# Optimization experiments

Hardware: AMD Instinct MI355X
Metric: run time of the kernel (lower is better)

The kernel has to match this reference:

```python
import jax, jax.numpy as jnp
import numpy as np

TOP_K = 8

def setup_inputs() -> dict:
    key = jax.random.key(0)
    k1, k2, k3, k4 = jax.random.split(key, 4)
    B, T, C, E = 4, 4096, 2048, 64
    x = jax.random.normal(k1, (B, T, C), dtype=jnp.float32)
    w_route = jax.random.normal(k2, (E, C), dtype=jnp.float32) * (C ** -0.5)
    w_noise = jax.random.normal(k3, (E, C), dtype=jnp.float32) * (C ** -0.5)
    noise = jax.random.normal(k4, (B, T, E), dtype=jnp.float32)
    return {"x": x, "w_route": w_route, "w_noise": w_noise, "noise": noise}

def reference(x, w_route, w_noise, noise):
    # logits = x @ W_route^T ; noise_logits = x @ W_noise^T  (bias-free Linears)
    logits = jnp.einsum('btc,ec->bte', x, w_route)
    noise_logits = jnp.einsum('btc,ec,->bte', x, w_noise, jnp.float32(1.0)) if False else jnp.einsum('btc,ec->bte', x, w_noise)
    noisy_logits = logits + noise * jax.nn.softplus(noise_logits)
    # top-k over experts, scatter into -inf tensor, then softmax
    topk_vals, indices = jax.lax.top_k(noisy_logits, TOP_K)  # (B,T,K)
    E = noisy_logits.shape[-1]
    in_topk = jax.nn.one_hot(indices, E, dtype=jnp.bool_).any(axis=-2)  # (B,T,E)
    sparse_logits = jnp.where(in_topk, noisy_logits, -jnp.inf)
    router_output = jax.nn.softmax(sparse_logits, axis=-1)
    return router_output, indices
```

## Files before the change

kernel.cpp:

```cpp
#include <hip/hip_runtime.h>
#include <math.h>


#define CDIM  2048
#define EDIM  64
#define NOUT  128
#define TOPK  8
#define BM    32
#define BKS   64
#define NSIT  (CDIM / BKS)
#define NKC   (CDIM / 32)
#define TAU   1e-3f
#define XPS   136

typedef __attribute__((ext_vector_type(8))) short bf16x8;
typedef __attribute__((ext_vector_type(4))) float f32x4;

__device__ __forceinline__ void split8(const float4 a, const float4 b,
                                       bf16x8& h8, bf16x8& l8) {
    const float vv[8] = {a.x, a.y, a.z, a.w, b.x, b.y, b.z, b.w};
    #pragma unroll
    for (int j = 0; j < 8; ++j) {
        const __bf16 h = (__bf16)vv[j];
        const __bf16 l = (__bf16)(vv[j] - (float)h);
        h8[j] = __builtin_bit_cast(short, h);
        l8[j] = __builtin_bit_cast(short, l);
    }
}

__global__ __launch_bounds__(256)
void convert_w(const float* __restrict__ wr, const float* __restrict__ wn,
               short* __restrict__ whi, short* __restrict__ wlo) {
    const int s    = (int)blockIdx.x * 256 + (int)threadIdx.x;
    const int lane = s & 63;
    const int cg   = (s >> 6) & 7;
    const int kc   = s >> 9;
    const int col  = cg * 16 + (lane & 15);
    const int k0   = kc * 32 + (lane >> 4) * 8;
    const float* src = (col < EDIM ? wr + (size_t)col * CDIM
                                   : wn + (size_t)(col - EDIM) * CDIM) + k0;
    const float4 a = *(const float4*)src;
    const float4 b = *(const float4*)(src + 4);
    bf16x8 h8, l8; split8(a, b, h8, l8);
    *(bf16x8*)(whi + (size_t)s * 8) = h8;
    *(bf16x8*)(wlo + (size_t)s * 8) = l8;
}

__global__ __launch_bounds__(256, 2)
void router_fused(const float* __restrict__ x,
                  const short* __restrict__ whi,
                  const short* __restrict__ wlo,
                  const float* __restrict__ w_route,
                  const float* __restrict__ w_noise,
                  const float* __restrict__ noise,
                  float* __restrict__ out_probs,
                  float* __restrict__ out_idx)
{
    __shared__ __align__(16) short xsh[2][BM][XPS];
    __shared__ __align__(16) float scr[BM][NOUT + 8];
    __shared__ __align__(16) float vals[4][64];
    __shared__ __align__(16) float srt[4][64];

    const int tid  = (int)threadIdx.x;
    const int lane = tid & 63;
    const int wid  = tid >> 6;
    const int wr   = wid >> 1;
    const int wc   = wid & 1;
    const int l15  = lane & 15;
    const int q8   = (lane >> 4) * 8;
    const int q4   = (lane >> 4) * 4;
    const int row0 = (int)blockIdx.x * BM;

    const int srow = tid >> 3;
    const int skk  = (tid & 7) * 8;
    const float* xsrc = x + (size_t)(row0 + srow) * CDIM + skk;

    f32x4 acc[4];
    #pragma unroll
    for (int nc = 0; nc < 4; ++nc)
        acc[nc] = (f32x4){0.f, 0.f, 0.f, 0.f};

    bf16x8 bh[2][4], bl[2][4];
    auto loadB = [&](int buf, int kc) {
        const int base = (kc * 8 + wc * 4) * 512 + lane * 8;
        #pragma unroll
        for (int nc = 0; nc < 4; ++nc) {
            bh[buf][nc] = *(const bf16x8*)(whi + base + nc * 512);
            bl[buf][nc] = *(const bf16x8*)(wlo + base + nc * 512);
        }
    };

    loadB(0, 0);
    {
        const float4 a = *(const float4*)xsrc;
        const float4 b = *(const float4*)(xsrc + 4);
        bf16x8 h8, l8; split8(a, b, h8, l8);
        *(bf16x8*)&xsh[0][srow][skk]      = h8;
        *(bf16x8*)&xsh[0][srow][64 + skk] = l8;
    }
    __syncthreads();

    #pragma unroll 2
    for (int sit = 0; sit < NSIT; ++sit) {
        const int  cur = sit & 1;
        const bool pf  = (sit + 1 < NSIT);
        const int  g0  = sit * 2;

        loadB(1, g0 + 1);
        float4 pa, pb;
        if (pf) {
            pa = *(const float4*)(xsrc + (sit + 1) * BKS);
            pb = *(const float4*)(xsrc + (sit + 1) * BKS + 4);
        }

        const short* ar = &xsh[cur][wr * 16 + l15][0];
        {
            const bf16x8 ah = *(const bf16x8*)(ar + q8);
            const bf16x8 al = *(const bf16x8*)(ar + 64 + q8);
            #pragma unroll
            for (int nc = 0; nc < 4; ++nc) {
                acc[nc] = __builtin_amdgcn_mfma_f32_16x16x32_bf16(ah, bh[0][nc], acc[nc], 0, 0, 0);
                acc[nc] = __builtin_amdgcn_mfma_f32_16x16x32_bf16(al, bh[0][nc], acc[nc], 0, 0, 0);
                acc[nc] = __builtin_amdgcn_mfma_f32_16x16x32_bf16(ah, bl[0][nc], acc[nc], 0, 0, 0);
            }
        }
        if (g0 + 2 < NKC) loadB(0, g0 + 2);
        {
            const bf16x8 ah = *(const bf16x8*)(ar + 32 + q8);
            const bf16x8 al = *(const bf16x8*)(ar + 96 + q8);
            #pragma unroll
            for (int nc = 0; nc < 4; ++nc) {
                acc[nc] = __builtin_amdgcn_mfma_f32_16x16x32_bf16(ah, bh[1][nc], acc[nc], 0, 0, 0);
                acc[nc] = __builtin_amdgcn_mfma_f32_16x16x32_bf16(al, bh[1][nc], acc[nc], 0, 0, 0);
                acc[nc] = __builtin_amdgcn_mfma_f32_16x16x32_bf16(ah, bl[1][nc], acc[nc], 0, 0, 0);
            }
        }
        if (pf) {
            bf16x8 h8, l8; split8(pa, pb, h8, l8);
            *(bf16x8*)&xsh[cur ^ 1][srow][skk]      = h8;
            *(bf16x8*)&xsh[cur ^ 1][srow][64 + skk] = l8;
        }
        __syncthreads();
    }

    #pragma unroll
    for (int nc = 0; nc < 4; ++nc)
        #pragma unroll
        for (int g = 0; g < 4; ++g)
            scr[wr * 16 + q4 + g][wc * 64 + nc * 16 + l15] = acc[nc][g];
    __syncthreads();

    #pragma unroll 1
    for (int r8 = 0; r8 < 8; ++r8) {
        const int row  = wid * 8 + r8;
        const int grow = row0 + row;

        const float route = scr[row][lane];
        const float nz    = scr[row][EDIM + lane];
        const float nv    = noise[(size_t)grow * EDIM + lane];
        const float sp = fmaxf(nz, 0.f) + log1pf(expf(-fabsf(nz)));
        const float nl = route + nv * sp;

        vals[wid][lane] = nl;
        __syncthreads();

        int cnt = 0;
        #pragma unroll
        for (int jq = 0; jq < 16; ++jq) {
            const float4 v = *(const float4*)&vals[wid][jq * 4];
            const int j0 = jq * 4;
            cnt += (v.x > nl || (v.x == nl && (j0 + 0) < lane));
            cnt += (v.y > nl || (v.y == nl && (j0 + 1) < lane));
            cnt += (v.z > nl || (v.z == nl && (j0 + 2) < lane));
            cnt += (v.w > nl || (v.w == nl && (j0 + 3) < lane));
        }
        srt[wid][cnt] = nl;
        __syncthreads();

        const float m = srt[wid][0];
        bool amb = false, flagme = false;
        float prev = m;
        #pragma unroll
        for (int t = 1; t <= TOPK; ++t) {
            const float vt = srt[wid][t];
            if (prev - vt < TAU) {
                amb = true;
                const float vb = 0.5f * (prev + vt);
                flagme = flagme || (fabsf(nl - vb) <= TAU);
            }
            prev = vt;
        }

        if (cnt < TOPK) out_idx[(size_t)grow * TOPK + cnt] = (float)lane;
        float ev = (cnt < TOPK) ? expf(nl - m) : 0.f;
        float s  = ev;
        #pragma unroll
        for (int off = 32; off >= 1; off >>= 1) s += __shfl_xor(s, off, 64);
        out_probs[(size_t)grow * EDIM + lane] = ev / s;

        if (amb) {
            unsigned long long mask = __ballot(flagme);
            double nld = (double)nl;
            const float* xr = x + (size_t)grow * CDIM;
            while (mask) {
                const int e = (int)__ffsll(mask) - 1;
                mask &= (mask - 1);
                double ar2 = 0.0, an = 0.0;
                const float* wrp = w_route + (size_t)e * CDIM;
                const float* wnp = w_noise + (size_t)e * CDIM;
                #pragma unroll
                for (int j = 0; j < 8; ++j) {
                    const int k = (j * 64 + lane) * 4;
                    const float4 xv = *(const float4*)(xr + k);
                    const float4 rv = *(const float4*)(wrp + k);
                    const float4 nq = *(const float4*)(wnp + k);
                    ar2 = fma((double)xv.x, (double)rv.x, ar2);
                    ar2 = fma((double)xv.y, (double)rv.y, ar2);
                    ar2 = fma((double)xv.z, (double)rv.z, ar2);
                    ar2 = fma((double)xv.w, (double)rv.w, ar2);
                    an  = fma((double)xv.x, (double)nq.x, an);
                    an  = fma((double)xv.y, (double)nq.y, an);
                    an  = fma((double)xv.z, (double)nq.z, an);
                    an  = fma((double)xv.w, (double)nq.w, an);
                }
                #pragma unroll
                for (int off = 32; off >= 1; off >>= 1) {
                    ar2 += __shfl_xor(ar2, off, 64);
                    an  += __shfl_xor(an, off, 64);
                }
                const double spd = fmax(an, 0.0) + log1p(exp(-fabs(an)));
                const double nve = (double)__shfl(nv, e, 64);
                const double v   = ar2 + nve * spd;
                if (lane == e) nld = v;
            }
            double workd = nld;
            int    rank2 = -1;
            double m2 = 0.0;
            #pragma unroll
            for (int t = 0; t < TOPK; ++t) {
                double bv = workd;
                int    bi = lane;
                #pragma unroll
                for (int off = 32; off >= 1; off >>= 1) {
                    const double ov = __shfl_xor(bv, off, 64);
                    const int    oi = __shfl_xor(bi, off, 64);
                    if (ov > bv || (ov == bv && oi < bi)) { bv = ov; bi = oi; }
                }
                if (t == 0) m2 = bv;
                if (lane == bi) {
                    rank2 = t;
                    workd = -INFINITY;
                    out_idx[(size_t)grow * TOPK + t] = (float)lane;
                }
            }
            float ev2 = (rank2 >= 0) ? expf((float)(nld - m2)) : 0.f;
            float s2  = ev2;
            #pragma unroll
            for (int off = 32; off >= 1; off >>= 1) s2 += __shfl_xor(s2, off, 64);
            out_probs[(size_t)grow * EDIM + lane] = ev2 / s2;
        }
    }
}

extern "C" void kernel_launch(void* const* d_in, const int* in_sizes, int n_in,
                              void* d_out, int out_size, void* d_ws, size_t ws_size,
                              hipStream_t stream)
{
    const float* x       = (const float*)d_in[0];
    const float* w_route = (const float*)d_in[1];
    const float* w_noise = (const float*)d_in[2];
    const float* noise   = (const float*)d_in[3];

    const int n_rows = in_sizes[0] / CDIM;
    float* out_probs = (float*)d_out;
    float* out_idx   = out_probs + (size_t)n_rows * EDIM;

    short* whi = (short*)d_ws;
    short* wlo = whi + (size_t)NOUT * CDIM;

    hipLaunchKernelGGL(convert_w, dim3(NOUT * CDIM / (256 * 8)), dim3(256), 0, stream,
                       w_route, w_noise, whi, wlo);
    hipLaunchKernelGGL(router_fused, dim3(n_rows / BM), dim3(256), 0, stream,
                       x, whi, wlo, w_route, w_noise, noise, out_probs, out_idx);
}
```

Baseline: 298.9 us.

## Double row tile to 512 threads, prefetch x two steps ahead, use wave-local syncs

Each block now covers 64 rows with 512 threads, where the old kernel used 32 rows and 256. Activation loads are issued two iterations ahead, and both B fragment sets are loaded at the start of each step. The score scratch buffer now reuses the x staging LDS, and the per-wave top-k phase replaces block barriers with lgkmcnt waits, since each wave only touches its own rows. This aims to hide global latency and cut barrier cost, but it raises register pressure and may lower occupancy. The wave-local syncs also rely on wave-level LDS ordering.

```diff
diff --git a/kernel.cpp b/kernel.cpp
--- a/kernel.cpp
+++ b/kernel.cpp
@@ -2,16 +2,17 @@
 #include <math.h>
 
 
-#define CDIM  2048
-#define EDIM  64
-#define NOUT  128
-#define TOPK  8
-#define BM    32
-#define BKS   64
-#define NSIT  (CDIM / BKS)
-#define NKC   (CDIM / 32)
-#define TAU   1e-3f
-#define XPS   136
+#define CDIM   2048
+#define EDIM   64
+#define NOUT   128
+#define TOPK   8
+#define NROWS  16384
+#define BM     64
+#define BK     64
+#define NIT    (CDIM / BK)
+#define TAU    1e-3f
+#define XPS    136
+#define SCP    132
 
 typedef __attribute__((ext_vector_type(8))) short bf16x8;
 typedef __attribute__((ext_vector_type(4))) float f32x4;
@@ -26,6 +27,15 @@
         h8[j] = __builtin_bit_cast(short, h);
         l8[j] = __builtin_bit_cast(short, l);
     }
+}
+
+__device__ __forceinline__ void block_sync() {
+    asm volatile("s_waitcnt lgkmcnt(0)" ::: "memory");
+    __builtin_amdgcn_s_barrier();
+}
+
+__device__ __forceinline__ void wave_lds_sync() {
+    asm volatile("s_waitcnt lgkmcnt(0)" ::: "memory");
 }
 
 __global__ __launch_bounds__(256)
@@ -46,7 +56,7 @@
     *(bf16x8*)(wlo + (size_t)s * 8) = l8;
 }
 
-__global__ __launch_bounds__(256, 2)
+__global__ __launch_bounds__(512)
 void router_fused(const float* __restrict__ x,
                   const short* __restrict__ whi,
                   const short* __restrict__ wlo,
@@ -57,9 +67,8 @@
                   float* __restrict__ out_idx)
 {
     __shared__ __align__(16) short xsh[2][BM][XPS];
-    __shared__ __align__(16) float scr[BM][NOUT + 8];
-    __shared__ __align__(16) float vals[4][64];
-    __shared__ __align__(16) float srt[4][64];
+    __shared__ float vals[8][64];
+    __shared__ float srt[8][64];
 
     const int tid  = (int)threadIdx.x;
     const int lane = tid & 63;
@@ -72,46 +81,54 @@
     const int row0 = (int)blockIdx.x * BM;
 
     const int srow = tid >> 3;
-    const int skk  = (tid & 7) * 8;
-    const float* xsrc = x + (size_t)(row0 + srow) * CDIM + skk;
+    const int soct = tid & 7;
+    const float* xsrc = x + (size_t)(row0 + srow) * CDIM + soct * 8;
 
     f32x4 acc[4];
     #pragma unroll
     for (int nc = 0; nc < 4; ++nc)
         acc[nc] = (f32x4){0.f, 0.f, 0.f, 0.f};
 
-    bf16x8 bh[2][4], bl[2][4];
-    auto loadB = [&](int buf, int kc) {
+    bf16x8 bh0[4], bl0[4], bh1[4], bl1[4];
+    auto loadB0 = [&](int kc) {
         const int base = (kc * 8 + wc * 4) * 512 + lane * 8;
         #pragma unroll
         for (int nc = 0; nc < 4; ++nc) {
-            bh[buf][nc] = *(const bf16x8*)(whi + base + nc * 512);
-            bl[buf][nc] = *(const bf16x8*)(wlo + base + nc * 512);
+            bh0[nc] = *(const bf16x8*)(whi + base + nc * 512);
+            bl0[nc] = *(const bf16x8*)(wlo + base + nc * 512);
         }
     };
-
-    loadB(0, 0);
-    {
-        const float4 a = *(const float4*)xsrc;
-        const float4 b = *(const float4*)(xsrc + 4);
-        bf16x8 h8, l8; split8(a, b, h8, l8);
-        *(bf16x8*)&xsh[0][srow][skk]      = h8;
-        *(bf16x8*)&xsh[0][srow][64 + skk] = l8;
-    }
-    __syncthreads();
+    auto loadB1 = [&](int kc) {
+        const int base = (kc * 8 + wc * 4) * 512 + lane * 8;
+        #pragma unroll
+        for (int nc = 0; nc < 4; ++nc) {
+            bh1[nc] = *(const bf16x8*)(whi + base + nc * 512);
+            bl1[nc] = *(const bf16x8*)(wlo + base + nc * 512);
+        }
+    };
+
+    float4 pf[2][2];
+    auto issue = [&](int slot, int it) {
+        pf[slot][0] = *(const float4*)(xsrc + it * BK);
+        pf[slot][1] = *(const float4*)(xsrc + it * BK + 4);
+    };
+    auto stage = [&](int buf, int slot) {
+        bf16x8 h8, l8; split8(pf[slot][0], pf[slot][1], h8, l8);
+        *(bf16x8*)&xsh[buf][srow][soct * 8]      = h8;
+        *(bf16x8*)&xsh[buf][srow][64 + soct * 8] = l8;
+    };
+
+    issue(0, 0);
+    stage(0, 0);
+    issue(1, 1);
+    block_sync();
 
     #pragma unroll 2
-    for (int sit = 0; sit < NSIT; ++sit) {
-        const int  cur = sit & 1;
-        const bool pf  = (sit + 1 < NSIT);
-        const int  g0  = sit * 2;
-
-        loadB(1, g0 + 1);
-        float4 pa, pb;
-        if (pf) {
-            pa = *(const float4*)(xsrc + (sit + 1) * BKS);
-            pb = *(const float4*)(xsrc + (sit + 1) * BKS + 4);
-        }
+    for (int it = 0; it < NIT; ++it) {
+        const int cur = it & 1;
+        loadB0(2 * it);
+        loadB1(2 * it + 1);
+        if (it + 2 < NIT) issue(cur, it + 2);
 
         const short* ar = &xsh[cur][wr * 16 + l15][0];
         {
@@ -119,50 +136,49 @@
             const bf16x8 al = *(const bf16x8*)(ar + 64 + q8);
             #pragma unroll
             for (int nc = 0; nc < 4; ++nc) {
-                acc[nc] = __builtin_amdgcn_mfma_f32_16x16x32_bf16(ah, bh[0][nc], acc[nc], 0, 0, 0);
-                acc[nc] = __builtin_amdgcn_mfma_f32_16x16x32_bf16(al, bh[0][nc], acc[nc], 0, 0, 0);
-                acc[nc] = __builtin_amdgcn_mfma_f32_16x16x32_bf16(ah, bl[0][nc], acc[nc], 0, 0, 0);
-            }
-        }
-        if (g0 + 2 < NKC) loadB(0, g0 + 2);
+                acc[nc] = __builtin_amdgcn_mfma_f32_16x16x32_bf16(ah, bh0[nc], acc[nc], 0, 0, 0);
+                acc[nc] = __builtin_amdgcn_mfma_f32_16x16x32_bf16(al, bh0[nc], acc[nc], 0, 0, 0);
+                acc[nc] = __builtin_amdgcn_mfma_f32_16x16x32_bf16(ah, bl0[nc], acc[nc], 0, 0, 0);
+            }
+        }
         {
             const bf16x8 ah = *(const bf16x8*)(ar + 32 + q8);
             const bf16x8 al = *(const bf16x8*)(ar + 96 + q8);
             #pragma unroll
             for (int nc = 0; nc < 4; ++nc) {
-                acc[nc] = __builtin_amdgcn_mfma_f32_16x16x32_bf16(ah, bh[1][nc], acc[nc], 0, 0, 0);
-                acc[nc] = __builtin_amdgcn_mfma_f32_16x16x32_bf16(al, bh[1][nc], acc[nc], 0, 0, 0);
-                acc[nc] = __builtin_amdgcn_mfma_f32_16x16x32_bf16(ah, bl[1][nc], acc[nc], 0, 0, 0);
-            }
-        }
-        if (pf) {
-            bf16x8 h8, l8; split8(pa, pb, h8, l8);
-            *(bf16x8*)&xsh[cur ^ 1][srow][skk]      = h8;
-            *(bf16x8*)&xsh[cur ^ 1][srow][64 + skk] = l8;
-        }
-        __syncthreads();
+                acc[nc] = __builtin_amdgcn_mfma_f32_16x16x32_bf16(ah, bh1[nc], acc[nc], 0, 0, 0);
+                acc[nc] = __builtin_amdgcn_mfma_f32_16x16x32_bf16(al, bh1[nc], acc[nc], 0, 0, 0);
+                acc[nc] = __builtin_amdgcn_mfma_f32_16x16x32_bf16(ah, bl1[nc], acc[nc], 0, 0, 0);
+            }
+        }
+        if (it + 1 < NIT) {
+            stage(cur ^ 1, cur ^ 1);
+            block_sync();
+        }
     }
 
+    __syncthreads();
+    float* scr = (float*)&xsh[0][0][0];
     #pragma unroll
     for (int nc = 0; nc < 4; ++nc)
         #pragma unroll
         for (int g = 0; g < 4; ++g)
-            scr[wr * 16 + q4 + g][wc * 64 + nc * 16 + l15] = acc[nc][g];
+            scr[(wr * 16 + q4 + g) * SCP + wc * 64 + nc * 16 + l15] = acc[nc][g];
     __syncthreads();
 
     #pragma unroll 1
-    for (int r8 = 0; r8 < 8; ++r8) {
-        const int row  = wid * 8 + r8;
+    for (int r = 0; r < 8; ++r) {
+        const int row  = wid * 8 + r;
         const int grow = row0 + row;
 
-        const float route = scr[row][lane];
-        const float nz    = scr[row][EDIM + lane];
+        const float route = scr[row * SCP + lane];
+        const float nz    = scr[row * SCP + 64 + lane];
         const float nv    = noise[(size_t)grow * EDIM + lane];
         const float sp = fmaxf(nz, 0.f) + log1pf(expf(-fabsf(nz)));
         const float nl = route + nv * sp;
 
         vals[wid][lane] = nl;
-        __syncthreads();
+        wave_lds_sync();
 
         int cnt = 0;
         #pragma unroll
@@ -175,7 +191,7 @@
             cnt += (v.w > nl || (v.w == nl && (j0 + 3) < lane));
         }
         srt[wid][cnt] = nl;
-        __syncthreads();
+        wave_lds_sync();
 
         const float m = srt[wid][0];
         bool amb = false, flagme = false;
@@ -280,6 +296,6 @@
 
     hipLaunchKernelGGL(convert_w, dim3(NOUT * CDIM / (256 * 8)), dim3(256), 0, stream,
                        w_route, w_noise, whi, wlo);
-    hipLaunchKernelGGL(router_fused, dim3(n_rows / BM), dim3(256), 0, stream,
+    hipLaunchKernelGGL(router_fused, dim3(n_rows / BM), dim3(512), 0, stream,
                        x, whi, wlo, w_route, w_noise, noise, out_probs, out_idx);
 }
```

Result: faster. 278.3 us (-6.9%).
